# Optimization experiments

Hardware: AMD Instinct MI355X
Metric: run time of the kernel (lower is better)

## Reference

```python
import jax, jax.numpy as jnp
import numpy as np

EPS = 1e-5

def _layernorm(x, g, b):
    mu = jnp.mean(x, axis=-1, keepdims=True)
    var = jnp.mean(jnp.square(x - mu), axis=-1, keepdims=True)
    return (x - mu) * jax.lax.rsqrt(var + EPS) * g + b

def setup_inputs() -> dict:
    S, B, D, H, F = 4096, 2, 512, 8, 2048
    key = jax.random.key(0)
    ks = jax.random.split(key, 10)
    sc = 0.02
    return {
        "src": jax.random.normal(ks[0], (S, B, D), jnp.float32),
        "qkv_w": jax.random.normal(ks[1], (3 * D, D), jnp.float32) * sc,
        "qkv_b": jnp.zeros((3 * D,), jnp.float32),
        "out_w": jax.random.normal(ks[2], (D, D), jnp.float32) * sc,
        "w1": jax.random.normal(ks[3], (F, D), jnp.float32) * sc,
        "b1": jnp.zeros((F,), jnp.float32),
        "w2": jax.random.normal(ks[4], (D, F), jnp.float32) * sc,
        "b2": jnp.zeros((D,), jnp.float32),
        "ln1_g": jnp.ones((D,), jnp.float32),
        "ln1_b": jnp.zeros((D,), jnp.float32),
        "ln2_g": jnp.ones((D,), jnp.float32),
        "ln2_b": jnp.zeros((D,), jnp.float32),
    }

def reference(src, qkv_w, qkv_b, out_w, w1, b1, w2, b2, ln1_g, ln1_b, ln2_g, ln2_b):
    S, B, D = src.shape
    H = 8
    hd = D // H
    # --- self attention (NOTE: no 1/sqrt(hd) scaling, matching source) ---
    qkv = src @ qkv_w.T + qkv_b                      # [S, B, 3D]
    q, k, v = jnp.split(qkv, 3, axis=-1)             # each [S, B, D]
    # [S, B*H, hd] -> [B*H, S, hd]
    q = q.reshape(S, B * H, hd).transpose(1, 0, 2)
    k = k.reshape(S, B * H, hd).transpose(1, 0, 2)
    v = v.reshape(S, B * H, hd).transpose(1, 0, 2)
    scores = jnp.einsum('nqd,nkd->nqk', q, k)        # [B*H, S, S]
    attn = jax.nn.softmax(scores, axis=-1)           # dropout = identity (eval)
    out = jnp.einsum('nqk,nkd->nqd', attn, v)        # [B*H, S, hd]
    out = out.transpose(1, 0, 2).reshape(S, B, D)
    attn_out = out @ out_w.T                         # out_proj has no bias
    # --- post-norm residual + FFN ---
    x = _layernorm(src + attn_out, ln1_g, ln1_b)
    ffn = jax.nn.relu(x @ w1.T + b1) @ w2.T + b2
    x = _layernorm(x + ffn, ln2_g, ln2_b)
    return x
```

## Files before the change

kernel.cpp:

```cpp
#include <hip/hip_runtime.h>
#include <cstdint>
#include <math.h>

#define CF4(p) (*reinterpret_cast<const float4*>(p))
#define F4(p)  (*reinterpret_cast<float4*>(p))

typedef __attribute__((ext_vector_type(8))) short bf16x8;
typedef __attribute__((ext_vector_type(4))) float f32x4;

__device__ __forceinline__ unsigned short f2bf(float x) {
  union { float f; unsigned int u; } v; v.f = x;
  unsigned int r = v.u + 0x7FFF + ((v.u >> 16) & 1);
  return (unsigned short)(r >> 16);
}

__device__ __forceinline__ int swz(int row, int col) {
  return row * 64 + (col ^ ((row & 7) << 3));
}

__device__ __forceinline__ void gload_lds16(const void* g, void* lds) {
  __builtin_amdgcn_global_load_lds(
      (const __attribute__((address_space(1))) void*)g,
      (__attribute__((address_space(3))) void*)lds, 16, 0, 0);
}

__global__ __launch_bounds__(256) void cvt_all_kernel(
    const float* __restrict__ src,   unsigned short* __restrict__ src_bf,
    const float* __restrict__ qkvw,  unsigned short* __restrict__ qkvw_bf,
    const float* __restrict__ outw,  unsigned short* __restrict__ outw_bf,
    const float* __restrict__ w1,    unsigned short* __restrict__ w1_bf,
    const float* __restrict__ w2,    unsigned short* __restrict__ w2_bf)
{
  int i = blockIdx.x * 256 + threadIdx.x;
  const float* s; unsigned short* d;
  if      (i < 524288) { s = src;  d = src_bf;                        }
  else if (i < 622592) { s = qkvw; d = qkvw_bf; i -= 524288;          }
  else if (i < 655360) { s = outw; d = outw_bf; i -= 622592;          }
  else if (i < 786432) { s = w1;   d = w1_bf;   i -= 655360;          }
  else if (i < 917504) { s = w2;   d = w2_bf;   i -= 786432;          }
  else return;
  float4 a = CF4(&s[i * 8]), b = CF4(&s[i * 8 + 4]);
  union { bf16x8 v; unsigned short u[8]; } w;
  w.u[0] = f2bf(a.x); w.u[1] = f2bf(a.y); w.u[2] = f2bf(a.z); w.u[3] = f2bf(a.w);
  w.u[4] = f2bf(b.x); w.u[5] = f2bf(b.y); w.u[6] = f2bf(b.z); w.u[7] = f2bf(b.w);
  *reinterpret_cast<bf16x8*>(&d[i * 8]) = w.v;
}

template<int BNT, int BIAS, int RELU, int RES, int OBF>
__global__ __launch_bounds__(256, 2) void bgemm_kernel(
    void* __restrict__ Cv, const unsigned short* __restrict__ A,
    const unsigned short* __restrict__ W, const float* __restrict__ bias,
    const float* __restrict__ R, int M, int N, int K)
{
  constexpr int NJ = BNT / 32;
  __shared__ __align__(16) unsigned short As[2][128 * 64];
  __shared__ __align__(16) unsigned short Ws[2][BNT * 64];

  const int t    = threadIdx.x;
  const int lane = t & 63, wid = t >> 6;
  const int g    = lane >> 4, lr = lane & 15;
  const int wm   = wid >> 1,  wn = wid & 1;
  const int m0   = blockIdx.y * 128, n0 = blockIdx.x * BNT;

  const int sr8 = lane >> 3;
  const int sc  = (lane & 7) ^ sr8;
  const unsigned short* Ag = A + (size_t)(m0 + sr8) * K + sc * 8;
  const unsigned short* Wg = W + (size_t)(n0 + sr8) * K + sc * 8;

  f32x4 acc[4][NJ];
#pragma unroll
  for (int mi = 0; mi < 4; ++mi)
#pragma unroll
    for (int nj = 0; nj < NJ; ++nj)
      acc[mi][nj] = (f32x4){0.f, 0.f, 0.f, 0.f};

#define STAGE_G(buf, k0)                                                   \
  {                                                                        \
    _Pragma("unroll")                                                      \
    for (int i = 0; i < 4; ++i) {                                          \
      const int rb = wid * 32 + i * 8;                                     \
      gload_lds16(Ag + (size_t)rb * K + (k0), (void*)&As[buf][rb * 64]);   \
    }                                                                      \
    _Pragma("unroll")                                                      \
    for (int i = 0; i < BNT / 32; ++i) {                                   \
      const int rb = wid * (BNT / 4) + i * 8;                              \
      gload_lds16(Wg + (size_t)rb * K + (k0), (void*)&Ws[buf][rb * 64]);   \
    }                                                                      \
  }

  STAGE_G(0, 0);
  __syncthreads();

  const int nk = K >> 6;
  for (int kt = 0; kt < nk; ++kt) {
    const int cur = kt & 1;
    if (kt + 1 < nk) STAGE_G(cur ^ 1, (kt + 1) * 64);
#pragma unroll
    for (int ks = 0; ks < 2; ++ks) {
      bf16x8 af[4], bfr[NJ];
#pragma unroll
      for (int mi = 0; mi < 4; ++mi) {
        const int row = wm * 64 + mi * 16 + lr;
        af[mi] = *reinterpret_cast<const bf16x8*>(
            &As[cur][row * 64 + (((ks * 4 + g) ^ (row & 7)) * 8)]);
      }
#pragma unroll
      for (int nj = 0; nj < NJ; ++nj) {
        const int row = wn * (BNT / 2) + nj * 16 + lr;
        bfr[nj] = *reinterpret_cast<const bf16x8*>(
            &Ws[cur][row * 64 + (((ks * 4 + g) ^ (row & 7)) * 8)]);
      }
#pragma unroll
      for (int mi = 0; mi < 4; ++mi)
#pragma unroll
        for (int nj = 0; nj < NJ; ++nj)
          acc[mi][nj] = __builtin_amdgcn_mfma_f32_16x16x32_bf16(
              bfr[nj], af[mi], acc[mi][nj], 0, 0, 0);
    }
    __syncthreads();
  }
#undef STAGE_G

#pragma unroll
  for (int mi = 0; mi < 4; ++mi) {
    const int r = m0 + wm * 64 + mi * 16 + lr;
#pragma unroll
    for (int nj = 0; nj < NJ; ++nj) {
      const int c0 = n0 + wn * (BNT / 2) + nj * 16 + g * 4;
      float4 v = make_float4(acc[mi][nj][0], acc[mi][nj][1],
                             acc[mi][nj][2], acc[mi][nj][3]);
      if (BIAS) {
        float4 bb = CF4(&bias[c0]);
        v.x += bb.x; v.y += bb.y; v.z += bb.z; v.w += bb.w;
      }
      if (RES) {
        float4 rr = CF4(&R[(size_t)r * N + c0]);
        v.x += rr.x; v.y += rr.y; v.z += rr.z; v.w += rr.w;
      }
      if (RELU) {
        v.x = fmaxf(v.x, 0.f); v.y = fmaxf(v.y, 0.f);
        v.z = fmaxf(v.z, 0.f); v.w = fmaxf(v.w, 0.f);
      }
      if (OBF) {
        unsigned int w0, w1;
        asm("v_cvt_pk_bf16_f32 %0, %1, %2" : "=v"(w0) : "v"(v.x), "v"(v.y));
        asm("v_cvt_pk_bf16_f32 %0, %1, %2" : "=v"(w1) : "v"(v.z), "v"(v.w));
        *reinterpret_cast<uint2*>(
            &((unsigned short*)Cv)[(size_t)r * N + c0]) = make_uint2(w0, w1);
      } else {
        F4(&((float*)Cv)[(size_t)r * N + c0]) = v;
      }
    }
  }
}

__global__ __launch_bounds__(256, 2) void attn_kernel(
    unsigned short* __restrict__ O, const unsigned short* __restrict__ qkv)
{
  const int Bb = 2, LD = 1536, DM = 512;
  const int qt = blockIdx.x;
  const int nh = blockIdx.y;
  const int b = nh >> 3, h = nh & 7;
  const int cq = h * 64, ck = 512 + h * 64, cv = 1024 + h * 64;

  __shared__ __align__(16) unsigned short Ks [2][64 * 64];
  __shared__ __align__(16) unsigned short Vts[2][64 * 64];
  __shared__ __align__(16) unsigned short Ps [128 * 64];

  const int t    = threadIdx.x;
  const int lane = t & 63;
  const int wid  = t >> 6;
  const int g    = lane >> 4;
  const int lr   = lane & 15;
  const int wq0  = wid * 32;

  bf16x8 qf[2][2];
#pragma unroll
  for (int mi = 0; mi < 2; ++mi)
#pragma unroll
    for (int kq = 0; kq < 2; ++kq)
      qf[mi][kq] = *reinterpret_cast<const bf16x8*>(
          &qkv[((size_t)(qt * 128 + wq0 + mi * 16 + lr) * Bb + b) * LD
               + cq + kq * 32 + g * 8]);

  f32x4 o_acc[2][4];
  float lsum[2] = {0.f, 0.f};
#pragma unroll
  for (int mi = 0; mi < 2; ++mi)
#pragma unroll
    for (int dj = 0; dj < 4; ++dj)
      o_acc[mi][dj] = (f32x4){0.f, 0.f, 0.f, 0.f};

  const int sr8 = lane >> 3;
  const int scK = (lane & 7) ^ sr8;
  const int vD0 = wid * 8;
  const int vSr = lane;

#define STAGE_K(buf, kt)                                               \
  {                                                                    \
    _Pragma("unroll")                                                  \
    for (int i = 0; i < 2; ++i) {                                      \
      const int rb = wid * 16 + i * 8;                                 \
      gload_lds16(&qkv[((size_t)((kt) * 64 + rb + sr8) * Bb + b) * LD  \
                       + ck + scK * 8],                                \
                  (void*)&Ks[buf][rb * 64]);                           \
    }                                                                  \
  }
#define LOAD_V(kt)                                                     \
  {                                                                    \
    _Pragma("unroll")                                                  \
    for (int p = 0; p < 2; ++p)                                        \
      vr[p] = *reinterpret_cast<const bf16x8*>(                        \
          &qkv[((size_t)((kt) * 64 + vSr) * Bb + b) * LD + cv          \
               + vD0 + p * 32]);                                       \
  }
#define WRITE_V(buf)                                                   \
  {                                                                    \
    _Pragma("unroll")                                                  \
    for (int p = 0; p < 2; ++p) {                                      \
      const int d0 = vD0 + p * 32;                                     \
      union { bf16x8 v; unsigned short u[8]; } w;                      \
      w.v = vr[p];                                                     \
      _Pragma("unroll")                                                \
      for (int j = 0; j < 8; ++j)                                      \
        Vts[buf][swz(d0 + j, vSr)] = w.u[j];                           \
    }                                                                  \
  }

  bf16x8 vr[2];
  STAGE_K(0, 0);
  LOAD_V(0);
  WRITE_V(0);
  __syncthreads();

  for (int kt = 0; kt < 64; ++kt) {
    const int cur = kt & 1;
    const bool hasNext = (kt < 63);
    if (hasNext) { STAGE_K(cur ^ 1, kt + 1); LOAD_V(kt + 1); }

    f32x4 sfT[2][4];
#pragma unroll
    for (int mi = 0; mi < 2; ++mi)
#pragma unroll
      for (int nj = 0; nj < 4; ++nj)
        sfT[mi][nj] = (f32x4){0.f, 0.f, 0.f, 0.f};
    __builtin_amdgcn_s_setprio(1);
#pragma unroll
    for (int nj = 0; nj < 4; ++nj) {
#pragma unroll
      for (int kq = 0; kq < 2; ++kq) {
        bf16x8 ak = *reinterpret_cast<const bf16x8*>(
            &Ks[cur][swz(nj * 16 + lr, kq * 32 + g * 8)]);
        sfT[0][nj] = __builtin_amdgcn_mfma_f32_16x16x32_bf16(
            ak, qf[0][kq], sfT[0][nj], 0, 0, 0);
        sfT[1][nj] = __builtin_amdgcn_mfma_f32_16x16x32_bf16(
            ak, qf[1][kq], sfT[1][nj], 0, 0, 0);
      }
    }
    __builtin_amdgcn_s_setprio(0);

#pragma unroll
    for (int mi = 0; mi < 2; ++mi) {
      const int qrow = wq0 + mi * 16 + lr;
#pragma unroll
      for (int nj = 0; nj < 4; ++nj) {
        const float p0 = __expf(sfT[mi][nj][0]);
        const float p1 = __expf(sfT[mi][nj][1]);
        const float p2 = __expf(sfT[mi][nj][2]);
        const float p3 = __expf(sfT[mi][nj][3]);
        lsum[mi] += (p0 + p1) + (p2 + p3);
        unsigned int w0, w1;
        asm("v_cvt_pk_bf16_f32 %0, %1, %2" : "=v"(w0) : "v"(p0), "v"(p1));
        asm("v_cvt_pk_bf16_f32 %0, %1, %2" : "=v"(w1) : "v"(p2), "v"(p3));
        *reinterpret_cast<uint2*>(&Ps[swz(qrow, nj * 16 + g * 4)]) =
            make_uint2(w0, w1);
      }
    }

    __builtin_amdgcn_s_setprio(1);
#pragma unroll
    for (int kks = 0; kks < 2; ++kks) {
      bf16x8 pa0 = *reinterpret_cast<const bf16x8*>(
          &Ps[swz(wq0 +  0 + lr, kks * 32 + g * 8)]);
      bf16x8 pa1 = *reinterpret_cast<const bf16x8*>(
          &Ps[swz(wq0 + 16 + lr, kks * 32 + g * 8)]);
#pragma unroll
      for (int dj = 0; dj < 4; ++dj) {
        bf16x8 vb = *reinterpret_cast<const bf16x8*>(
            &Vts[cur][swz(dj * 16 + lr, kks * 32 + g * 8)]);
        o_acc[0][dj] = __builtin_amdgcn_mfma_f32_16x16x32_bf16(
            pa0, vb, o_acc[0][dj], 0, 0, 0);
        o_acc[1][dj] = __builtin_amdgcn_mfma_f32_16x16x32_bf16(
            pa1, vb, o_acc[1][dj], 0, 0, 0);
      }
    }
    __builtin_amdgcn_s_setprio(0);

    if (hasNext) WRITE_V(cur ^ 1);
    __syncthreads();
  }
#undef STAGE_K
#undef LOAD_V
#undef WRITE_V

#pragma unroll
  for (int mi = 0; mi < 2; ++mi) {
    float rs = lsum[mi];
    rs += __shfl_xor(rs, 16);
    rs += __shfl_xor(rs, 32);
#pragma unroll
    for (int reg = 0; reg < 4; ++reg) {
      const float rsq = __shfl(rs, (lane & 48) + g * 4 + reg);
      const float inv = 1.f / rsq;
      const int q = qt * 128 + wq0 + mi * 16 + g * 4 + reg;
#pragma unroll
      for (int dj = 0; dj < 4; ++dj)
        O[((size_t)q * Bb + b) * DM + h * 64 + dj * 16 + lr] =
            f2bf(o_acc[mi][dj][reg] * inv);
    }
  }
}

template<int WBF>
__global__ __launch_bounds__(256) void ln_kernel(
    float* __restrict__ out, unsigned short* __restrict__ obf,
    const float* __restrict__ in, const float* __restrict__ g,
    const float* __restrict__ bb)
{
  const int w = threadIdx.x >> 6, lane = threadIdx.x & 63;
  const size_t row = (size_t)blockIdx.x * 4 + w;
  const float* xr = in + row * 512;
  float4 v0 = CF4(&xr[lane * 4]);
  float4 v1 = CF4(&xr[256 + lane * 4]);
  float s = v0.x + v0.y + v0.z + v0.w + v1.x + v1.y + v1.z + v1.w;
  float q = v0.x*v0.x + v0.y*v0.y + v0.z*v0.z + v0.w*v0.w
          + v1.x*v1.x + v1.y*v1.y + v1.z*v1.z + v1.w*v1.w;
#pragma unroll
  for (int off = 1; off < 64; off <<= 1) {
    s += __shfl_xor(s, off);
    q += __shfl_xor(q, off);
  }
  const float mu  = s * (1.f / 512.f);
  const float var = q * (1.f / 512.f) - mu * mu;
  const float rst = rsqrtf(var + 1e-5f);
  float4 g0 = CF4(&g[lane * 4]),  g1 = CF4(&g[256 + lane * 4]);
  float4 b0 = CF4(&bb[lane * 4]), b1 = CF4(&bb[256 + lane * 4]);
  float* orow = out + row * 512;
  float4 o0, o1;
  o0.x = (v0.x - mu) * rst * g0.x + b0.x;
  o0.y = (v0.y - mu) * rst * g0.y + b0.y;
  o0.z = (v0.z - mu) * rst * g0.z + b0.z;
  o0.w = (v0.w - mu) * rst * g0.w + b0.w;
  o1.x = (v1.x - mu) * rst * g1.x + b1.x;
  o1.y = (v1.y - mu) * rst * g1.y + b1.y;
  o1.z = (v1.z - mu) * rst * g1.z + b1.z;
  o1.w = (v1.w - mu) * rst * g1.w + b1.w;
  F4(&orow[lane * 4]) = o0;
  F4(&orow[256 + lane * 4]) = o1;
  if (WBF) {
    unsigned short* brow = obf + row * 512;
    ushort4 u0 = make_ushort4(f2bf(o0.x), f2bf(o0.y), f2bf(o0.z), f2bf(o0.w));
    ushort4 u1 = make_ushort4(f2bf(o1.x), f2bf(o1.y), f2bf(o1.z), f2bf(o1.w));
    *reinterpret_cast<ushort4*>(&brow[lane * 4]) = u0;
    *reinterpret_cast<ushort4*>(&brow[256 + lane * 4]) = u1;
  }
}

extern "C" void kernel_launch(void* const* d_in, const int* in_sizes, int n_in,
                              void* d_out, int out_size, void* d_ws, size_t ws_size,
                              hipStream_t stream)
{
  const float* src   = (const float*)d_in[0];
  const float* qkv_w = (const float*)d_in[1];
  const float* qkv_b = (const float*)d_in[2];
  const float* out_w = (const float*)d_in[3];
  const float* w1    = (const float*)d_in[4];
  const float* b1    = (const float*)d_in[5];
  const float* w2    = (const float*)d_in[6];
  const float* b2    = (const float*)d_in[7];
  const float* ln1g  = (const float*)d_in[8];
  const float* ln1b  = (const float*)d_in[9];
  const float* ln2g  = (const float*)d_in[10];
  const float* ln2b  = (const float*)d_in[11];
  float* out = (float*)d_out;

  const int M = 8192;

  char* ws = (char*)d_ws;
  unsigned short* qkv_bf  = (unsigned short*)(ws + 0);
  unsigned short* attn_bf = (unsigned short*)(ws + 25165824);
  unsigned short* h_bf    = (unsigned short*)(ws + 0);
  float*          y       = (float*)(ws + 33554432);
  float*          z       = (float*)(ws + 33554432);
  float*          x       = (float*)(ws + 50331648);
  unsigned short* x_bf    = (unsigned short*)(ws + 67108864);
  unsigned short* src_bf  = (unsigned short*)(ws + 75497472);
  unsigned short* wqkv_bf = (unsigned short*)(ws + 83886080);
  unsigned short* wout_bf = (unsigned short*)(ws + 85458944);
  unsigned short* w1_bf   = (unsigned short*)(ws + 85983232);
  unsigned short* w2_bf   = (unsigned short*)(ws + 88080384);
  if (ws_size < (size_t)90177536) return;

  dim3 blk(256);

  cvt_all_kernel<<<dim3(3584), blk, 0, stream>>>(
      src, src_bf, qkv_w, wqkv_bf, out_w, wout_bf, w1, w1_bf, w2, w2_bf);

  bgemm_kernel<128,1,0,0,1><<<dim3(12, 64), blk, 0, stream>>>(
      qkv_bf, src_bf, wqkv_bf, qkv_b, nullptr, M, 1536, 512);
  attn_kernel<<<dim3(32, 16), blk, 0, stream>>>(attn_bf, qkv_bf);
  bgemm_kernel<64,0,0,1,0><<<dim3(8, 64), blk, 0, stream>>>(
      y, attn_bf, wout_bf, nullptr, src, M, 512, 512);
  ln_kernel<1><<<dim3(M / 4), blk, 0, stream>>>(x, x_bf, y, ln1g, ln1b);
  bgemm_kernel<128,1,1,0,1><<<dim3(16, 64), blk, 0, stream>>>(
      h_bf, x_bf, w1_bf, b1, nullptr, M, 2048, 512);
  bgemm_kernel<64,1,0,1,0><<<dim3(8, 64), blk, 0, stream>>>(
      z, h_bf, w2_bf, b2, x, M, 512, 2048);
  ln_kernel<0><<<dim3(M / 4), blk, 0, stream>>>(out, nullptr, z, ln2g, ln2b);
}
```

Measured before the change: 336.5 us.

## Prefetch two K-tiles ahead in GEMM with explicit vmcnt waits and barriers

The GEMM main loop now issues loads for two stages up front. Each iteration waits with a partial s_waitcnt vmcnt so only the current tile must have landed, then refills the freed buffer with tile kt+2 after the compute barrier. This lets global-to-LDS loads overlap more with MFMA work. The MFMA operand order is also swapped, which transposes the accumulator layout, so the epilogue writes scalar elements instead of float4 and converts to bf16 with a software rounding helper instead of packed cvt. That makes the stores narrower and less coalesced.

```diff
diff --git a/kernel.cpp b/kernel.cpp
--- a/kernel.cpp
+++ b/kernel.cpp
@@ -53,6 +53,7 @@
     const float* __restrict__ R, int M, int N, int K)
 {
   constexpr int NJ = BNT / 32;
+  constexpr int VM = 4 + BNT / 32;
   __shared__ __align__(16) unsigned short As[2][128 * 64];
   __shared__ __align__(16) unsigned short Ws[2][BNT * 64];
 
@@ -88,13 +89,19 @@
     }                                                                      \
   }
 
+  const int nk = K >> 6;
   STAGE_G(0, 0);
-  __syncthreads();
-
-  const int nk = K >> 6;
+  STAGE_G(1, 64);
+
   for (int kt = 0; kt < nk; ++kt) {
     const int cur = kt & 1;
-    if (kt + 1 < nk) STAGE_G(cur ^ 1, (kt + 1) * 64);
+    if (kt + 1 < nk) {
+      asm volatile("s_waitcnt vmcnt(%0)" :: "i"(VM) : "memory");
+    } else {
+      asm volatile("s_waitcnt vmcnt(0)" ::: "memory");
+    }
+    __builtin_amdgcn_s_barrier();
+
 #pragma unroll
     for (int ks = 0; ks < 2; ++ks) {
       bf16x8 af[4], bfr[NJ];
@@ -115,40 +122,28 @@
 #pragma unroll
         for (int nj = 0; nj < NJ; ++nj)
           acc[mi][nj] = __builtin_amdgcn_mfma_f32_16x16x32_bf16(
-              bfr[nj], af[mi], acc[mi][nj], 0, 0, 0);
-    }
-    __syncthreads();
+              af[mi], bfr[nj], acc[mi][nj], 0, 0, 0);
+    }
+
+    __builtin_amdgcn_s_barrier();
+    if (kt + 2 < nk) STAGE_G(cur, (kt + 2) * 64);
   }
 #undef STAGE_G
 
 #pragma unroll
   for (int mi = 0; mi < 4; ++mi) {
-    const int r = m0 + wm * 64 + mi * 16 + lr;
-#pragma unroll
-    for (int nj = 0; nj < NJ; ++nj) {
-      const int c0 = n0 + wn * (BNT / 2) + nj * 16 + g * 4;
-      float4 v = make_float4(acc[mi][nj][0], acc[mi][nj][1],
-                             acc[mi][nj][2], acc[mi][nj][3]);
-      if (BIAS) {
-        float4 bb = CF4(&bias[c0]);
-        v.x += bb.x; v.y += bb.y; v.z += bb.z; v.w += bb.w;
-      }
-      if (RES) {
-        float4 rr = CF4(&R[(size_t)r * N + c0]);
-        v.x += rr.x; v.y += rr.y; v.z += rr.z; v.w += rr.w;
-      }
-      if (RELU) {
-        v.x = fmaxf(v.x, 0.f); v.y = fmaxf(v.y, 0.f);
-        v.z = fmaxf(v.z, 0.f); v.w = fmaxf(v.w, 0.f);
-      }
-      if (OBF) {
-        unsigned int w0, w1;
-        asm("v_cvt_pk_bf16_f32 %0, %1, %2" : "=v"(w0) : "v"(v.x), "v"(v.y));
-        asm("v_cvt_pk_bf16_f32 %0, %1, %2" : "=v"(w1) : "v"(v.z), "v"(v.w));
-        *reinterpret_cast<uint2*>(
-            &((unsigned short*)Cv)[(size_t)r * N + c0]) = make_uint2(w0, w1);
-      } else {
-        F4(&((float*)Cv)[(size_t)r * N + c0]) = v;
+#pragma unroll
+    for (int reg = 0; reg < 4; ++reg) {
+      const int r = m0 + wm * 64 + mi * 16 + g * 4 + reg;
+#pragma unroll
+      for (int nj = 0; nj < NJ; ++nj) {
+        const int cc = n0 + wn * (BNT / 2) + nj * 16 + lr;
+        float v = acc[mi][nj][reg];
+        if (BIAS) v += bias[cc];
+        if (RES)  v += R[(size_t)r * N + cc];
+        if (RELU) v = fmaxf(v, 0.f);
+        if (OBF)  ((unsigned short*)Cv)[(size_t)r * N + cc] = f2bf(v);
+        else      ((float*)Cv)[(size_t)r * N + cc] = v;
       }
     }
   }
```

After: 323.9 us. 1.04x faster.
